# Kernel tuning notes

Hardware: AMD Instinct MI355X
Metric: run time of the kernel (lower is better)

## Reference

```python
import jax, jax.numpy as jnp
import numpy as np

N_PROJ, N_SP, D, H = 400000, 40000, 256, 8
DH = D // H  # 32
EPS = 1e-5
NEG_SLOPE = 0.2  # GATv2Conv default


def layer_norm(x, g, b):
    m = x.mean(-1, keepdims=True)
    v = ((x - m) ** 2).mean(-1, keepdims=True)
    return (x - m) / jnp.sqrt(v + EPS) * g + b


def setup_inputs() -> dict:
    key = jax.random.key(0)
    ks = jax.random.split(key, 8)
    w = lambda k, shape: jax.random.normal(k, shape, jnp.float32) * 0.05
    return dict(
        proj_features=jax.random.normal(ks[0], (N_PROJ, D), jnp.float32),
        prev_scenepoint_features=jax.random.normal(ks[1], (N_SP, D), jnp.float32),
        Wl=w(ks[2], (D, D)), bl=jnp.zeros((D,), jnp.float32),
        Wr=w(ks[3], (D, D)), br=jnp.zeros((D,), jnp.float32),
        att=w(ks[4], (H, DH)), gat_bias=jnp.zeros((D,), jnp.float32),
        ln1_g=jnp.ones((D,), jnp.float32), ln1_b=jnp.zeros((D,), jnp.float32),
        ln2_g=jnp.ones((D,), jnp.float32), ln2_b=jnp.zeros((D,), jnp.float32),
        mlp_W=w(ks[5], (D, D)), mlp_b=jnp.zeros((D,), jnp.float32),
        edge_src=jnp.arange(N_PROJ, dtype=jnp.int32),
        edge_tgt=jax.random.randint(ks[6], (N_PROJ,), 0, N_SP, jnp.int32),
    )


def reference(proj_features, prev_scenepoint_features, Wl, bl, Wr, br, att,
              gat_bias, ln1_g, ln1_b, ln2_g, ln2_b, mlp_W, mlp_b,
              edge_src, edge_tgt):
    # norm_and_proj_scenepoint2proj: LayerNorm + ReLU (no Linear: dims equal)
    x_agg = jax.nn.relu(layer_norm(prev_scenepoint_features, ln1_g, ln1_b))

    # GATv2Conv: lin_l on source (projection) nodes, lin_r on target (scene point) nodes
    xl = (proj_features @ Wl + bl).reshape(N_PROJ, H, DH)   # [Np,H,DH]
    xr = (x_agg @ Wr + br).reshape(N_SP, H, DH)             # [Ns,H,DH]
    xl_e = xl[edge_src]                                     # [E,H,DH]
    xr_e = xr[edge_tgt]                                     # [E,H,DH]
    e = jnp.einsum('ehd,hd->eh', jax.nn.leaky_relu(xl_e + xr_e, NEG_SLOPE), att)

    # segment softmax over edges sharing the same target scene point
    e_max = jax.ops.segment_max(e, edge_tgt, num_segments=N_SP)
    ex = jnp.exp(e - e_max[edge_tgt])
    denom = jax.ops.segment_sum(ex, edge_tgt, num_segments=N_SP)
    alpha = ex / (denom[edge_tgt] + 1e-16)                  # [E,H]

    out = jax.ops.segment_sum(alpha[..., None] * xl_e, edge_tgt, num_segments=N_SP)
    x = out.reshape(N_SP, D) + gat_bias                     # concat heads + bias

    # stateful residual with previous scene point features
    x = prev_scenepoint_features + x
    x_skip = x
    # norm_pre_mlp + ReLU, then mlp (single Linear since n_hidden_layers=0)
    x = jax.nn.relu(layer_norm(x, ln2_g, ln2_b))
    x = x @ mlp_W + mlp_b
    return x_skip + x
```

## Files before the change

### kernel.cpp

```cpp
#include <hip/hip_runtime.h>
#include <hip/hip_bf16.h>

#define D_DIM 256
#define EPS_LN 1e-5f
#define NEG_SLOPE 0.2f

typedef __bf16 bf16x8 __attribute__((ext_vector_type(8)));
typedef unsigned short ushortx8 __attribute__((ext_vector_type(8)));
typedef unsigned short ushortx4 __attribute__((ext_vector_type(4)));
typedef float floatx4 __attribute__((ext_vector_type(4)));

__device__ inline unsigned short f2bf(float f) {
    __hip_bfloat16 h = __float2bfloat16(f);
    return __builtin_bit_cast(unsigned short, h);
}
__device__ inline float bf2f(unsigned short u) {
    unsigned int x = ((unsigned int)u) << 16;
    return __builtin_bit_cast(float, x);
}

__device__ __forceinline__ void async_copy16(const void* g, void* l) {
    __builtin_amdgcn_global_load_lds(
        (const __attribute__((address_space(1))) unsigned int*)g,
        (__attribute__((address_space(3))) unsigned int*)l, 16, 0, 0);
}

__device__ inline bf16x8 cvt_frag(float4 a, float4 b) {
    ushortx8 u;
    u[0] = f2bf(a.x); u[1] = f2bf(a.y); u[2] = f2bf(a.z); u[3] = f2bf(a.w);
    u[4] = f2bf(b.x); u[5] = f2bf(b.y); u[6] = f2bf(b.z); u[7] = f2bf(b.w);
    return __builtin_bit_cast(bf16x8, u);
}

__global__ __launch_bounds__(256) void wtrans_kernel(
        const float* __restrict__ W0, const float* __restrict__ W1,
        const float* __restrict__ W2, unsigned short* __restrict__ T0,
        unsigned short* __restrict__ T1, unsigned short* __restrict__ T2) {
    const float* W = (blockIdx.y == 0) ? W0 : (blockIdx.y == 1) ? W1 : W2;
    unsigned short* T = (blockIdx.y == 0) ? T0 : (blockIdx.y == 1) ? T1 : T2;
    __shared__ float lds[64][65];
    const int tx = blockIdx.x & 3;
    const int ty = blockIdx.x >> 2;
    const int t = threadIdx.x;
    const int r = t >> 6;
    const int c = t & 63;
#pragma unroll
    for (int i = 0; i < 16; ++i) {
        int row = ty * 64 + r + i * 4;
        lds[r + i * 4][c] = W[row * 256 + tx * 64 + c];
    }
    __syncthreads();
#pragma unroll
    for (int i = 0; i < 16; ++i) {
        int orow = tx * 64 + r + i * 4;
        T[orow * 256 + ty * 64 + c] = f2bf(lds[c][r + i * 4]);
    }
}

__global__ __launch_bounds__(256) void ln_relu_kernel(
        const float* __restrict__ x, const float* __restrict__ g,
        const float* __restrict__ b, float* __restrict__ y, int nrows) {
    int row = blockIdx.x * 4 + (threadIdx.x >> 6);
    if (row >= nrows) return;
    int lane = threadIdx.x & 63;
    float4 v = ((const float4*)(x + (size_t)row * D_DIM))[lane];
    float s = v.x + v.y + v.z + v.w;
    float s2 = v.x * v.x + v.y * v.y + v.z * v.z + v.w * v.w;
#pragma unroll
    for (int m = 32; m >= 1; m >>= 1) {
        s += __shfl_xor(s, m, 64);
        s2 += __shfl_xor(s2, m, 64);
    }
    float mean = s * (1.f / D_DIM);
    float var = s2 * (1.f / D_DIM) - mean * mean;
    float rstd = rsqrtf(var + EPS_LN);
    float4 gv = ((const float4*)g)[lane];
    float4 bv = ((const float4*)b)[lane];
    float4 o;
    o.x = fmaxf((v.x - mean) * rstd * gv.x + bv.x, 0.f);
    o.y = fmaxf((v.y - mean) * rstd * gv.y + bv.y, 0.f);
    o.z = fmaxf((v.z - mean) * rstd * gv.z + bv.z, 0.f);
    o.w = fmaxf((v.w - mean) * rstd * gv.w + bv.w, 0.f);
    ((float4*)(y + (size_t)row * D_DIM))[lane] = o;
}

template <int OUT_BF16, int HAS_RES>
__global__ __launch_bounds__(256, 3) void gemm256_kernel(
        const float* __restrict__ A, const unsigned short* __restrict__ Wt,
        const float* __restrict__ bias, const float* __restrict__ res,
        void* __restrict__ out, int M) {
    __shared__ float As[2][128 * 32];
    __shared__ unsigned short Bs[2][128 * 32];
    const int n0 = blockIdx.x * 128;
    const int m0 = blockIdx.y * 128;
    const int t = threadIdx.x;
    const int lane = t & 63;
    const int wave = t >> 6;
    const int q = lane >> 4;
    const int l16 = lane & 15;
    const int wm = (wave & 1) * 64;
    const int wn = (wave >> 1) * 64;

    const int rowLA = lane >> 3;
    const int GA = (lane & 7) ^ (rowLA & 7);
    const int rowLB = lane >> 2;
    const int GB = (lane & 3) ^ ((lane >> 3) & 3);

    auto stage = [&](int buf, int kt) {
#pragma unroll
        for (int i = 0; i < 4; ++i) {
            int s = wave * 4 + i;
            int row = m0 + s * 8 + rowLA;
            row = row < M ? row : (M - 1);
            async_copy16(A + (size_t)row * 256 + kt * 32 + GA * 4,
                         &As[buf][s * 256]);
        }
#pragma unroll
        for (int i = 0; i < 2; ++i) {
            int s = wave * 2 + i;
            int row = n0 + s * 16 + rowLB;
            async_copy16(Wt + (size_t)row * 256 + kt * 32 + GB * 8,
                         &Bs[buf][s * 512]);
        }
    };

    floatx4 acc[4][4] = {};

    stage(0, 0);
    __syncthreads();

    for (int kt = 0; kt < 8; ++kt) {
        const int cur = kt & 1;
        if (kt < 7) stage(cur ^ 1, kt + 1);
        bf16x8 af[4], bfr[4];
#pragma unroll
        for (int mi = 0; mi < 4; ++mi) {
            int r = wm + mi * 16 + l16;
            int P0 = (2 * q) ^ (r & 7);
            float4 f0 = *(const float4*)&As[cur][r * 32 + P0 * 4];
            float4 f1 = *(const float4*)&As[cur][r * 32 + (P0 ^ 1) * 4];
            af[mi] = cvt_frag(f0, f1);
        }
#pragma unroll
        for (int ni = 0; ni < 4; ++ni) {
            int r = wn + ni * 16 + l16;
            int P = q ^ ((r >> 1) & 3);
            bfr[ni] = __builtin_bit_cast(bf16x8,
                *(const ushortx8*)&Bs[cur][r * 32 + P * 8]);
        }
#pragma unroll
        for (int mi = 0; mi < 4; ++mi)
#pragma unroll
            for (int ni = 0; ni < 4; ++ni)
                acc[mi][ni] = __builtin_amdgcn_mfma_f32_16x16x32_bf16(
                    af[mi], bfr[ni], acc[mi][ni], 0, 0, 0);
        __syncthreads();
    }

#pragma unroll
    for (int mi = 0; mi < 4; ++mi) {
#pragma unroll
        for (int ni = 0; ni < 4; ++ni) {
            int col = n0 + wn + ni * 16 + l16;
            float bcol = bias[col];
#pragma unroll
            for (int r = 0; r < 4; ++r) {
                int row = m0 + wm + mi * 16 + q * 4 + r;
                if (row < M) {
                    float v = acc[mi][ni][r] + bcol;
                    if (HAS_RES) v += res[(size_t)row * 256 + col];
                    if (OUT_BF16)
                        ((unsigned short*)out)[(size_t)row * 256 + col] = f2bf(v);
                    else
                        ((float*)out)[(size_t)row * 256 + col] = v;
                }
            }
        }
    }
}

__global__ void hist_kernel(const int* __restrict__ tgt, int* __restrict__ counts, int E) {
    int i = blockIdx.x * 256 + threadIdx.x;
    if (i < E) atomicAdd(&counts[tgt[i]], 1);
}

__global__ __launch_bounds__(1024) void scan_kernel(
        const int* __restrict__ counts, int* __restrict__ offs, int n) {
    __shared__ int lds[1024];
    int t = threadIdx.x;
    int CH = (n + 1023) >> 10;
    int beg = t * CH, end = min(beg + CH, n);
    int s = 0;
    for (int i = beg; i < end; ++i) s += counts[i];
    lds[t] = s;
    __syncthreads();
    for (int off = 1; off < 1024; off <<= 1) {
        int v = (t >= off) ? lds[t - off] : 0;
        __syncthreads();
        lds[t] += v;
        __syncthreads();
    }
    int run = lds[t] - s;
    for (int i = beg; i < end; ++i) { offs[i] = run; run += counts[i]; }
    if (t == 1023) offs[n] = lds[1023];
}

__global__ void scatter_kernel(const int* __restrict__ tgt, const int* __restrict__ src,
                               const int* __restrict__ offs, int* __restrict__ cursor,
                               int* __restrict__ slist, int E) {
    int i = blockIdx.x * 256 + threadIdx.x;
    if (i < E) {
        int tg = tgt[i];
        int p = atomicAdd(&cursor[tg], 1);
        slist[offs[tg] + p] = src[i];
    }
}

__global__ __launch_bounds__(256) void aggregate_kernel(
        const unsigned short* __restrict__ xl, const float* __restrict__ xr,
        const float* __restrict__ prev, const int* __restrict__ slist,
        const int* __restrict__ offs, const float* __restrict__ att,
        const float* __restrict__ gbias, const float* __restrict__ g2,
        const float* __restrict__ b2, float* __restrict__ x_skip,
        float* __restrict__ h2, int nsp) {
    int tgt = blockIdx.x * 4 + (threadIdx.x >> 6);
    if (tgt >= nsp) return;
    int lane = threadIdx.x & 63;
    float4 xrv = ((const float4*)(xr + (size_t)tgt * D_DIM))[lane];
    float4 attv = ((const float4*)att)[lane];
    float acc0 = 0.f, acc1 = 0.f, acc2 = 0.f, acc3 = 0.f, den = 0.f;
    int beg = offs[tgt], end = offs[tgt + 1];

    ushortx4 row = {};
    if (beg < end) {
        int src = slist[beg];
        row = ((const ushortx4*)(xl + (size_t)src * D_DIM))[lane];
    }
    for (int i = beg; i < end; ++i) {
        ushortx4 row_n = {};
        if (i + 1 < end) {
            int s1 = slist[i + 1];
            row_n = ((const ushortx4*)(xl + (size_t)s1 * D_DIM))[lane];
        }
        float x0 = bf2f(row[0]), x1 = bf2f(row[1]), x2 = bf2f(row[2]), x3 = bf2f(row[3]);
        float t0 = x0 + xrv.x, t1 = x1 + xrv.y, t2 = x2 + xrv.z, t3 = x3 + xrv.w;
        t0 = t0 > 0.f ? t0 : NEG_SLOPE * t0;
        t1 = t1 > 0.f ? t1 : NEG_SLOPE * t1;
        t2 = t2 > 0.f ? t2 : NEG_SLOPE * t2;
        t3 = t3 > 0.f ? t3 : NEG_SLOPE * t3;
        float p = t0 * attv.x + t1 * attv.y + t2 * attv.z + t3 * attv.w;
        p += __shfl_xor(p, 1, 64);
        p += __shfl_xor(p, 2, 64);
        p += __shfl_xor(p, 4, 64);
        float ex = __expf(p);
        den += ex;
        acc0 += ex * x0; acc1 += ex * x1; acc2 += ex * x2; acc3 += ex * x3;
        row = row_n;
    }
    float rden = 1.f / (den + 1e-16f);
    float4 pv = ((const float4*)(prev + (size_t)tgt * D_DIM))[lane];
    float4 gb = ((const float4*)gbias)[lane];
    float v0 = pv.x + acc0 * rden + gb.x;
    float v1 = pv.y + acc1 * rden + gb.y;
    float v2 = pv.z + acc2 * rden + gb.z;
    float v3 = pv.w + acc3 * rden + gb.w;
    float s = v0 + v1 + v2 + v3;
    float s2 = v0 * v0 + v1 * v1 + v2 * v2 + v3 * v3;
#pragma unroll
    for (int m = 32; m >= 1; m >>= 1) {
        s += __shfl_xor(s, m, 64);
        s2 += __shfl_xor(s2, m, 64);
    }
    float mean = s * (1.f / D_DIM);
    float var = s2 * (1.f / D_DIM) - mean * mean;
    float rstd = rsqrtf(var + EPS_LN);
    float4 g2v = ((const float4*)g2)[lane];
    float4 b2v = ((const float4*)b2)[lane];
    float4 xs; xs.x = v0; xs.y = v1; xs.z = v2; xs.w = v3;
    ((float4*)(x_skip + (size_t)tgt * D_DIM))[lane] = xs;
    float4 h;
    h.x = fmaxf((v0 - mean) * rstd * g2v.x + b2v.x, 0.f);
    h.y = fmaxf((v1 - mean) * rstd * g2v.y + b2v.y, 0.f);
    h.z = fmaxf((v2 - mean) * rstd * g2v.z + b2v.z, 0.f);
    h.w = fmaxf((v3 - mean) * rstd * g2v.w + b2v.w, 0.f);
    ((float4*)(h2 + (size_t)tgt * D_DIM))[lane] = h;
}

extern "C" void kernel_launch(void* const* d_in, const int* in_sizes, int n_in,
                              void* d_out, int out_size, void* d_ws, size_t ws_size,
                              hipStream_t stream) {
    const float* proj = (const float*)d_in[0];
    const float* prev = (const float*)d_in[1];
    const float* Wl   = (const float*)d_in[2];
    const float* bl   = (const float*)d_in[3];
    const float* Wr   = (const float*)d_in[4];
    const float* br   = (const float*)d_in[5];
    const float* att  = (const float*)d_in[6];
    const float* gbias= (const float*)d_in[7];
    const float* ln1g = (const float*)d_in[8];
    const float* ln1b = (const float*)d_in[9];
    const float* ln2g = (const float*)d_in[10];
    const float* ln2b = (const float*)d_in[11];
    const float* Wm   = (const float*)d_in[12];
    const float* mb   = (const float*)d_in[13];
    const int* esrc   = (const int*)d_in[14];
    const int* etgt   = (const int*)d_in[15];

    const int NP = in_sizes[0] / D_DIM;
    const int NS = in_sizes[1] / D_DIM;
    const int E  = in_sizes[14];

    char* base = (char*)d_ws;
    size_t off = 0;
    auto carve = [&](size_t bytes) {
        char* p = base + off;
        off += (bytes + 255) & ~(size_t)255;
        return p;
    };
    unsigned short* xl    = (unsigned short*)carve((size_t)NP * D_DIM * 2);
    float* x_agg          = (float*)carve((size_t)NS * D_DIM * 4);
    float* xr             = (float*)carve((size_t)NS * D_DIM * 4);
    float* x_skip         = (float*)carve((size_t)NS * D_DIM * 4);
    float* h2             = (float*)carve((size_t)NS * D_DIM * 4);
    unsigned short* Wt_l  = (unsigned short*)carve((size_t)D_DIM * D_DIM * 2);
    unsigned short* Wt_r  = (unsigned short*)carve((size_t)D_DIM * D_DIM * 2);
    unsigned short* Wt_m  = (unsigned short*)carve((size_t)D_DIM * D_DIM * 2);
    int* counts           = (int*)carve((size_t)NS * 4 * 2);
    int* cursor           = counts + NS;
    int* offs             = (int*)carve((size_t)(NS + 1) * 4);
    int* slist            = (int*)carve((size_t)E * 4);

    hipMemsetAsync(counts, 0, (size_t)NS * 4 * 2, stream);

    wtrans_kernel<<<dim3(16, 3), 256, 0, stream>>>(Wl, Wr, Wm, Wt_l, Wt_r, Wt_m);

    ln_relu_kernel<<<(NS + 3) / 4, 256, 0, stream>>>(prev, ln1g, ln1b, x_agg, NS);

    gemm256_kernel<0, 0><<<dim3(2, (NS + 127) / 128), 256, 0, stream>>>(
        x_agg, Wt_r, br, nullptr, (void*)xr, NS);

    gemm256_kernel<1, 0><<<dim3(2, (NP + 127) / 128), 256, 0, stream>>>(
        proj, Wt_l, bl, nullptr, (void*)xl, NP);

    hist_kernel<<<(E + 255) / 256, 256, 0, stream>>>(etgt, counts, E);
    scan_kernel<<<1, 1024, 0, stream>>>(counts, offs, NS);
    scatter_kernel<<<(E + 255) / 256, 256, 0, stream>>>(etgt, esrc, offs, cursor, slist, E);

    aggregate_kernel<<<(NS + 3) / 4, 256, 0, stream>>>(
        xl, xr, prev, slist, offs, att, gbias, ln2g, ln2b, x_skip, h2, NS);

    gemm256_kernel<0, 1><<<dim3(2, (NS + 127) / 128), 256, 0, stream>>>(
        h2, Wt_m, mb, x_skip, d_out, NS);
}
```

Before: 971.8 us.

## Widen GEMM tile to full N=256, stage epilogue through LDS, prefetch aggregate indices

Each GEMM block now computes a 128x256 output tile, covering the full N=256 width. The A rows are therefore read from global memory once instead of twice across two N-blocks, and the launch grid becomes 1-D. The epilogue stages results through shared memory so global stores and residual loads become coalesced float4 row writes. The aggregate kernel loads the source index two edges ahead to break the index-then-row dependency chain. The cost is doubled accumulator registers, 64KB of LDS and lower occupancy (launch bounds 2), which may reduce latency hiding.

```diff
diff --git a/kernel.cpp b/kernel.cpp
--- a/kernel.cpp
+++ b/kernel.cpp
@@ -85,46 +85,51 @@
 }
 
 template <int OUT_BF16, int HAS_RES>
-__global__ __launch_bounds__(256, 3) void gemm256_kernel(
+__global__ __launch_bounds__(256, 2) void gemm256_kernel(
         const float* __restrict__ A, const unsigned short* __restrict__ Wt,
         const float* __restrict__ bias, const float* __restrict__ res,
         void* __restrict__ out, int M) {
-    __shared__ float As[2][128 * 32];
-    __shared__ unsigned short Bs[2][128 * 32];
-    const int n0 = blockIdx.x * 128;
-    const int m0 = blockIdx.y * 128;
+    __shared__ __attribute__((aligned(16))) char smem[65536];
+    float* Asb = (float*)smem;
+    unsigned short* Bsb = (unsigned short*)(smem + 32768);
+    const int m0 = blockIdx.x * 128;
     const int t = threadIdx.x;
     const int lane = t & 63;
     const int wave = t >> 6;
     const int q = lane >> 4;
     const int l16 = lane & 15;
     const int wm = (wave & 1) * 64;
-    const int wn = (wave >> 1) * 64;
+    const int wn = (wave >> 1) * 128;
 
     const int rowLA = lane >> 3;
     const int GA = (lane & 7) ^ (rowLA & 7);
     const int rowLB = lane >> 2;
     const int GB = (lane & 3) ^ ((lane >> 3) & 3);
 
+    int arow[4];
+#pragma unroll
+    for (int i = 0; i < 4; ++i) {
+        int rr = m0 + (wave * 4 + i) * 8 + rowLA;
+        arow[i] = rr < M ? rr : (M - 1);
+    }
+
     auto stage = [&](int buf, int kt) {
 #pragma unroll
         for (int i = 0; i < 4; ++i) {
             int s = wave * 4 + i;
-            int row = m0 + s * 8 + rowLA;
-            row = row < M ? row : (M - 1);
-            async_copy16(A + (size_t)row * 256 + kt * 32 + GA * 4,
-                         &As[buf][s * 256]);
-        }
-#pragma unroll
-        for (int i = 0; i < 2; ++i) {
-            int s = wave * 2 + i;
-            int row = n0 + s * 16 + rowLB;
+            async_copy16(A + (size_t)arow[i] * 256 + kt * 32 + GA * 4,
+                         Asb + buf * 4096 + s * 256);
+        }
+#pragma unroll
+        for (int i = 0; i < 4; ++i) {
+            int s = wave * 4 + i;
+            int row = s * 16 + rowLB;
             async_copy16(Wt + (size_t)row * 256 + kt * 32 + GB * 8,
-                         &Bs[buf][s * 512]);
+                         Bsb + buf * 8192 + s * 512);
         }
     };
 
-    floatx4 acc[4][4] = {};
+    floatx4 acc[4][8] = {};
 
     stage(0, 0);
     __syncthreads();
@@ -132,47 +137,91 @@
     for (int kt = 0; kt < 8; ++kt) {
         const int cur = kt & 1;
         if (kt < 7) stage(cur ^ 1, kt + 1);
-        bf16x8 af[4], bfr[4];
+        bf16x8 af[4];
 #pragma unroll
         for (int mi = 0; mi < 4; ++mi) {
             int r = wm + mi * 16 + l16;
             int P0 = (2 * q) ^ (r & 7);
-            float4 f0 = *(const float4*)&As[cur][r * 32 + P0 * 4];
-            float4 f1 = *(const float4*)&As[cur][r * 32 + (P0 ^ 1) * 4];
+            const float* base = Asb + cur * 4096 + r * 32;
+            float4 f0 = *(const float4*)(base + P0 * 4);
+            float4 f1 = *(const float4*)(base + (P0 ^ 1) * 4);
             af[mi] = cvt_frag(f0, f1);
         }
-#pragma unroll
-        for (int ni = 0; ni < 4; ++ni) {
+        bf16x8 bfr[8];
+#pragma unroll
+        for (int ni = 0; ni < 8; ++ni) {
             int r = wn + ni * 16 + l16;
             int P = q ^ ((r >> 1) & 3);
             bfr[ni] = __builtin_bit_cast(bf16x8,
-                *(const ushortx8*)&Bs[cur][r * 32 + P * 8]);
+                *(const ushortx8*)(Bsb + cur * 8192 + r * 32 + P * 8));
         }
 #pragma unroll
         for (int mi = 0; mi < 4; ++mi)
 #pragma unroll
-            for (int ni = 0; ni < 4; ++ni)
+            for (int ni = 0; ni < 8; ++ni)
                 acc[mi][ni] = __builtin_amdgcn_mfma_f32_16x16x32_bf16(
                     af[mi], bfr[ni], acc[mi][ni], 0, 0, 0);
         __syncthreads();
     }
 
-#pragma unroll
-    for (int mi = 0; mi < 4; ++mi) {
-#pragma unroll
-        for (int ni = 0; ni < 4; ++ni) {
-            int col = n0 + wn + ni * 16 + l16;
-            float bcol = bias[col];
-#pragma unroll
-            for (int r = 0; r < 4; ++r) {
-                int row = m0 + wm + mi * 16 + q * 4 + r;
-                if (row < M) {
-                    float v = acc[mi][ni][r] + bcol;
-                    if (HAS_RES) v += res[(size_t)row * 256 + col];
-                    if (OUT_BF16)
-                        ((unsigned short*)out)[(size_t)row * 256 + col] = f2bf(v);
-                    else
-                        ((float*)out)[(size_t)row * 256 + col] = v;
+    if (OUT_BF16) {
+        unsigned short (*Cs)[256] = (unsigned short(*)[256])smem;
+#pragma unroll
+        for (int mi = 0; mi < 4; ++mi)
+#pragma unroll
+            for (int ni = 0; ni < 8; ++ni) {
+                int col = wn + ni * 16 + l16;
+                float bcol = bias[col];
+#pragma unroll
+                for (int r = 0; r < 4; ++r) {
+                    int row = wm + mi * 16 + q * 4 + r;
+                    Cs[row][col] = f2bf(acc[mi][ni][r] + bcol);
+                }
+            }
+        __syncthreads();
+        unsigned short* po = (unsigned short*)out;
+#pragma unroll
+        for (int it = 0; it < 16; ++it) {
+            int idx = it * 256 + t;
+            int row = idx >> 5;
+            int c = idx & 31;
+            if (m0 + row < M)
+                ((float4*)(po + (size_t)(m0 + row) * 256))[c] =
+                    ((const float4*)&Cs[row][0])[c];
+        }
+    } else {
+        float (*Cf)[256] = (float(*)[256])smem;
+        float* po = (float*)out;
+#pragma unroll
+        for (int h = 0; h < 2; ++h) {
+            __syncthreads();
+            if (wm == h * 64) {
+#pragma unroll
+                for (int mi = 0; mi < 4; ++mi)
+#pragma unroll
+                    for (int ni = 0; ni < 8; ++ni) {
+                        int col = wn + ni * 16 + l16;
+                        float bcol = bias[col];
+#pragma unroll
+                        for (int r = 0; r < 4; ++r)
+                            Cf[mi * 16 + q * 4 + r][col] =
+                                acc[mi][ni][r] + bcol;
+                    }
+            }
+            __syncthreads();
+#pragma unroll
+            for (int it = 0; it < 16; ++it) {
+                int idx = it * 256 + t;
+                int row = idx >> 6;
+                int c = idx & 63;
+                int grow = m0 + h * 64 + row;
+                if (grow < M) {
+                    float4 v = ((const float4*)&Cf[row][0])[c];
+                    if (HAS_RES) {
+                        float4 rv = ((const float4*)(res + (size_t)grow * 256))[c];
+                        v.x += rv.x; v.y += rv.y; v.z += rv.z; v.w += rv.w;
+                    }
+                    ((float4*)(po + (size_t)grow * 256))[c] = v;
                 }
             }
         }
@@ -232,16 +281,17 @@
     int beg = offs[tgt], end = offs[tgt + 1];
 
     ushortx4 row = {};
+    int src_n = 0;
     if (beg < end) {
         int src = slist[beg];
         row = ((const ushortx4*)(xl + (size_t)src * D_DIM))[lane];
+        if (beg + 1 < end) src_n = slist[beg + 1];
     }
     for (int i = beg; i < end; ++i) {
+        int src_n2 = (i + 2 < end) ? slist[i + 2] : 0;
         ushortx4 row_n = {};
-        if (i + 1 < end) {
-            int s1 = slist[i + 1];
-            row_n = ((const ushortx4*)(xl + (size_t)s1 * D_DIM))[lane];
-        }
+        if (i + 1 < end)
+            row_n = ((const ushortx4*)(xl + (size_t)src_n * D_DIM))[lane];
         float x0 = bf2f(row[0]), x1 = bf2f(row[1]), x2 = bf2f(row[2]), x3 = bf2f(row[3]);
         float t0 = x0 + xrv.x, t1 = x1 + xrv.y, t2 = x2 + xrv.z, t3 = x3 + xrv.w;
         t0 = t0 > 0.f ? t0 : NEG_SLOPE * t0;
@@ -255,7 +305,7 @@
         float ex = __expf(p);
         den += ex;
         acc0 += ex * x0; acc1 += ex * x1; acc2 += ex * x2; acc3 += ex * x3;
-        row = row_n;
+        row = row_n; src_n = src_n2;
     }
     float rden = 1.f / (den + 1e-16f);
     float4 pv = ((const float4*)(prev + (size_t)tgt * D_DIM))[lane];
@@ -336,10 +386,10 @@
 
     ln_relu_kernel<<<(NS + 3) / 4, 256, 0, stream>>>(prev, ln1g, ln1b, x_agg, NS);
 
-    gemm256_kernel<0, 0><<<dim3(2, (NS + 127) / 128), 256, 0, stream>>>(
+    gemm256_kernel<0, 0><<<(NS + 127) / 128, 256, 0, stream>>>(
         x_agg, Wt_r, br, nullptr, (void*)xr, NS);
 
-    gemm256_kernel<1, 0><<<dim3(2, (NP + 127) / 128), 256, 0, stream>>>(
+    gemm256_kernel<1, 0><<<(NP + 127) / 128, 256, 0, stream>>>(
         proj, Wt_l, bl, nullptr, (void*)xl, NP);
 
     hist_kernel<<<(E + 255) / 256, 256, 0, stream>>>(etgt, counts, E);
@@ -349,6 +399,6 @@
     aggregate_kernel<<<(NS + 3) / 4, 256, 0, stream>>>(
         xl, xr, prev, slist, offs, att, gbias, ln2g, ln2b, x_skip, h2, NS);
 
-    gemm256_kernel<0, 1><<<dim3(2, (NS + 127) / 128), 256, 0, stream>>>(
+    gemm256_kernel<0, 1><<<(NS + 127) / 128, 256, 0, stream>>>(
         h2, Wt_m, mb, x_skip, d_out, NS);
 }
```

Measured after the change: 916.2 us. 5.7% less time.
